# Performance work log

Hardware: AMD Instinct MI355X
Metric: run time of the kernel (lower is better)

## Reference

```python
import jax, jax.numpy as jnp
import numpy as np

B, S, T, H, VS, VT = 64, 64, 64, 1024, 32000, 32000


def _init(key, shape, scale=0.05):
    return scale * jax.random.normal(key, shape, dtype=jnp.float32)


def setup_inputs() -> dict:
    key = jax.random.key(0)
    ks = jax.random.split(key, 16)
    source = jax.random.randint(ks[0], (B, S), 0, VS)
    target = jax.random.randint(ks[1], (B, T), 0, VT)
    emb_src = _init(ks[2], (VS, H)).at[0].set(0.0)   # padding_idx=0
    emb_tgt = _init(ks[3], (VT, H)).at[0].set(0.0)   # padding_idx=0
    W_ih_enc = _init(ks[4], (4 * H, H)); W_hh_enc = _init(ks[5], (4 * H, H))
    b_ih_enc = _init(ks[6], (4 * H,));   b_hh_enc = _init(ks[7], (4 * H,))
    W_ih_dec = _init(ks[8], (4 * H, H)); W_hh_dec = _init(ks[9], (4 * H, H))
    b_ih_dec = _init(ks[10], (4 * H,));  b_hh_dec = _init(ks[11], (4 * H,))
    W_att = _init(ks[12], (H, 2 * H));   b_att = _init(ks[13], (H,))
    W_out = _init(ks[14], (VT, H));      b_out = _init(ks[15], (VT,))
    return dict(source=source, target=target, emb_src=emb_src, emb_tgt=emb_tgt,
                W_ih_enc=W_ih_enc, W_hh_enc=W_hh_enc, b_ih_enc=b_ih_enc, b_hh_enc=b_hh_enc,
                W_ih_dec=W_ih_dec, W_hh_dec=W_hh_dec, b_ih_dec=b_ih_dec, b_hh_dec=b_hh_dec,
                W_att=W_att, b_att=b_att, W_out=W_out, b_out=b_out)


def _lstm_cell(x, h, c, W_ih, W_hh, b):
    # PyTorch gate order: i, f, g, o
    gates = x @ W_ih.T + h @ W_hh.T + b
    i, f, g, o = jnp.split(gates, 4, axis=-1)
    c_new = jax.nn.sigmoid(f) * c + jax.nn.sigmoid(i) * jnp.tanh(g)
    h_new = jax.nn.sigmoid(o) * jnp.tanh(c_new)
    return h_new, c_new


def reference(source, target, emb_src, emb_tgt,
              W_ih_enc, W_hh_enc, b_ih_enc, b_hh_enc,
              W_ih_dec, W_hh_dec, b_ih_dec, b_hh_dec,
              W_att, b_att, W_out, b_out):
    src = source.T              # [S, B]
    tgt = target.T              # [T, B]
    h0 = jnp.zeros((B, H), jnp.float32)
    c0 = jnp.zeros((B, H), jnp.float32)

    # ---- Encoder: time-major LSTM via scan (dropout in eval mode = identity) ----
    x_src = emb_src[src]        # [S, B, H]
    b_enc = b_ih_enc + b_hh_enc

    def enc_step(carry, x_t):
        h, c = carry
        h, c = _lstm_cell(x_t, h, c, W_ih_enc, W_hh_enc, b_enc)
        return (h, c), h

    (hT, cT), hx_list = jax.lax.scan(enc_step, (h0, c0), x_src)  # hx_list: [S, B, H]

    # ---- Decoder: hx_cx is never updated in the original loop, so every
    # timestep uses the SAME encoder final state -> fully vectorizable over t ----
    words_f = tgt[: S - 1]      # [Td, B], Td = T-1 (S == T)
    words_t = tgt[1:]           # [Td, B]
    x_dec = emb_tgt[words_f]    # [Td, B, H]
    b_dec = b_ih_dec + b_hh_dec
    gates = x_dec @ W_ih_dec.T + (hT @ W_hh_dec.T + b_dec)[None]  # [Td, B, 4H]
    i, f, g, o = jnp.split(gates, 4, axis=-1)
    c_new = jax.nn.sigmoid(f) * cT[None] + jax.nn.sigmoid(i) * jnp.tanh(g)
    hx = jax.nn.sigmoid(o) * jnp.tanh(c_new)                       # [Td, B, H]

    # ---- Attention (dot-product over source positions, softmax over S) ----
    scores = jnp.einsum('tbh,sbh->tsb', hx, hx_list)               # [Td, S, B]
    neg_inf = jnp.asarray(-jnp.inf, jnp.float32)
    mask = (src != 0)[None]                                        # [1, S, B]
    scores = jnp.where(mask, scores, neg_inf)
    align = jax.nn.softmax(scores, axis=1)                         # over S
    content = jnp.einsum('tsb,sbh->tbh', align, hx_list)           # [Td, B, H]
    concat = jnp.concatenate([content, hx], axis=-1)               # [Td, B, 2H]
    hx_att = jnp.tanh(concat @ W_att.T + b_att)                    # [Td, B, H]

    # ---- Output projection + per-step cross entropy (ignore_index=0), summed ----
    logits = hx_att @ W_out.T + b_out                              # [Td, B, VT]
    logp = jax.nn.log_softmax(logits, axis=-1)
    nll = -jnp.take_along_axis(logp, words_t[..., None], axis=-1).squeeze(-1)  # [Td, B]
    valid = (words_t != 0).astype(jnp.float32)
    per_step = jnp.sum(nll * valid, axis=1) / jnp.maximum(jnp.sum(valid, axis=1), 1.0)
    return jnp.sum(per_step)
```

## Files before the change

kernel.cpp:

```cpp
#include <hip/hip_runtime.h>
#include <math.h>

#define Bb 64
#define Ss 64
#define Hh 1024
#define Vv 32000
#define RD 4032
#define RP 4096
#define NT4 4096
#define ENC_NBLK 128

typedef unsigned short u16;
typedef unsigned long long u64;
typedef __attribute__((ext_vector_type(8))) short bf16x8;
typedef __attribute__((ext_vector_type(4))) float f32x4;

#define MFMA(a, b, c) __builtin_amdgcn_mfma_f32_16x16x32_bf16(a, b, c, 0, 0, 0)

__device__ __forceinline__ u16 f2b(float f) {
  union { float f; unsigned u; } v; v.f = f;
  unsigned r = v.u + 0x7fffu + ((v.u >> 16) & 1u);
  return (u16)(r >> 16);
}
__device__ __forceinline__ float b2f(u16 b) {
  union { unsigned u; float f; } v; v.u = ((unsigned)b) << 16; return v.f;
}
__device__ __forceinline__ float sigf(float x) { return 1.f / (1.f + expf(-x)); }

__device__ __forceinline__ void gll16(const void* g, void* l) {
  __builtin_amdgcn_global_load_lds(
      (const __attribute__((address_space(1))) unsigned int*)g,
      (__attribute__((address_space(3))) unsigned int*)l, 16, 0, 0);
}

__global__ void k_fail(float* out) { out[0] = 1e30f; }

__global__ void k_cvt(const float* __restrict__ in, u16* __restrict__ out, int n4) {
  int i = blockIdx.x * blockDim.x + threadIdx.x;
  const int st = gridDim.x * blockDim.x;
  for (; i < n4; i += st) {
    float4 v = ((const float4*)in)[i];
    ushort4 o; o.x = f2b(v.x); o.y = f2b(v.y); o.z = f2b(v.z); o.w = f2b(v.w);
    ((ushort4*)out)[i] = o;
  }
}

__global__ void k_gather(const int* __restrict__ tok, const float* __restrict__ emb,
                         u16* __restrict__ outp, int nstep) {
  const int r = blockIdx.x;
  const int step = r >> 6, b = r & 63;
  const int idx = (step < nstep) ? tok[b * 64 + step] : 0;
  const float4 v = ((const float4*)(emb + (size_t)idx * Hh))[threadIdx.x];
  ushort4 o; o.x = f2b(v.x); o.y = f2b(v.y); o.z = f2b(v.z); o.w = f2b(v.w);
  ((ushort4*)(outp + (size_t)r * Hh))[threadIdx.x] = o;
}

template<int EPI>
__global__ __launch_bounds__(256)
void k_gemm(const u16* __restrict__ A, const u16* __restrict__ Bm,
            float* __restrict__ C, int M, int N, int K,
            const float* __restrict__ bias, int act,
            float* __restrict__ pmax, float* __restrict__ psum, int ncols) {
  __shared__ __align__(16) u16 As[128 * 64];
  __shared__ __align__(16) u16 Bs[128 * 64];
  const int tid = threadIdx.x;
  const int wave = tid >> 6, lane = tid & 63;
  const int l15 = lane & 15, lhi = lane >> 4;
  int bx = blockIdx.x, by = blockIdx.y;
  {
    const int nwg = gridDim.x * gridDim.y;
    if ((nwg & 7) == 0) {
      int flat = by * gridDim.x + bx;
      const int q = nwg >> 3;
      flat = (flat & 7) * q + (flat >> 3);
      bx = flat % gridDim.x; by = flat / gridDim.x;
    }
  }
  const int m0 = by * 128, n0 = bx * 128;
  const int wm = (wave >> 1) * 64, wn = (wave & 1) * 64;
  f32x4 acc[4][4] = {};

  const int srow = wave * 32 + (lane >> 3);
  const int scolb = (lane & 7) * 16;

  for (int k0 = 0; k0 < K; k0 += 64) {
    __syncthreads();
#pragma unroll
    for (int q = 0; q < 4; ++q) {
      const int r = srow + q * 8;
      int ra = m0 + r; ra = (ra < M) ? ra : (M - 1);
      const char* ga = (const char*)(A + (size_t)ra * K + k0) + scolb;
      const char* gb = (const char*)(Bm + (size_t)(n0 + r) * K + k0) + scolb;
      char* lA = (char*)As + (wave * 32 + q * 8) * 128;
      char* lB = (char*)Bs + (wave * 32 + q * 8) * 128;
      gll16(ga, lA);
      gll16(gb, lB);
    }
    __syncthreads();
#pragma unroll
    for (int kk = 0; kk < 2; ++kk) {
      const int ko = kk * 32 + lhi * 8;
      bf16x8 af[4], bfr[4];
#pragma unroll
      for (int i = 0; i < 4; ++i) af[i] = *(const bf16x8*)(As + (wm + i * 16 + l15) * 64 + ko);
#pragma unroll
      for (int j = 0; j < 4; ++j) bfr[j] = *(const bf16x8*)(Bs + (wn + j * 16 + l15) * 64 + ko);
#pragma unroll
      for (int i = 0; i < 4; ++i)
#pragma unroll
        for (int j = 0; j < 4; ++j)
          acc[i][j] = MFMA(af[i], bfr[j], acc[i][j]);
    }
  }

  if (EPI == 0) {
#pragma unroll
    for (int i = 0; i < 4; ++i) {
      const int gr = m0 + wm + i * 16 + lhi * 4;
#pragma unroll
      for (int j = 0; j < 4; ++j) {
        const int gc = n0 + wn + j * 16 + l15;
        const float bv = bias ? bias[gc] : 0.f;
#pragma unroll
        for (int rr = 0; rr < 4; ++rr) {
          float v = acc[i][j][rr] + bv;
          if (act) v = tanhf(v);
          C[(size_t)(gr + rr) * N + gc] = v;
        }
      }
    }
  } else {
    float bj[4];
#pragma unroll
    for (int j = 0; j < 4; ++j) bj[j] = bias[n0 + wn + j * 16 + l15];
    const int pc = bx * 2 + (wn ? 1 : 0);
#pragma unroll
    for (int i = 0; i < 4; ++i) {
#pragma unroll
      for (int rr = 0; rr < 4; ++rr) {
        float v0 = acc[i][0][rr] + bj[0];
        float v1 = acc[i][1][rr] + bj[1];
        float v2 = acc[i][2][rr] + bj[2];
        float v3 = acc[i][3][rr] + bj[3];
        float m = fmaxf(fmaxf(v0, v1), fmaxf(v2, v3));
#pragma unroll
        for (int d = 1; d < 16; d <<= 1) m = fmaxf(m, __shfl_xor(m, d, 64));
        float s = __expf(v0 - m) + __expf(v1 - m) + __expf(v2 - m) + __expf(v3 - m);
#pragma unroll
        for (int d = 1; d < 16; d <<= 1) s += __shfl_xor(s, d, 64);
        if (l15 == 0) {
          const int grow = m0 + wm + i * 16 + lhi * 4 + rr;
          pmax[(size_t)grow * ncols + pc] = m;
          psum[(size_t)grow * ncols + pc] = s;
        }
      }
    }
  }
}

__global__ __launch_bounds__(256, 1)
void k_enc_all(const u16* __restrict__ Wb, const float* __restrict__ gx,
               const float* __restrict__ b_ih, const float* __restrict__ b_hh,
               u16* __restrict__ hxl, float* __restrict__ c_out, int* flags) {
  __shared__ __align__(16) u16 Ws[32 * 1024];
  __shared__ float Gs[64 * 33];
  __shared__ float Cs[512];
  __shared__ float bsum[32];
  const int tid = threadIdx.x;
  const int wave = tid >> 6, lane = tid & 63;
  const int l15 = lane & 15, lhi = lane >> 4;
  const int c0 = blockIdx.x * 8;
  const int cb = tid >> 2, hp = (tid & 3) * 2;

  for (int i = tid; i < 32 * 128; i += 256) {
    const int rr = i >> 7, ck = i & 127;
    const int wrow = (rr >> 3) * Hh + c0 + (rr & 7);
    const int bo = (ck * 16) ^ ((rr & 7) << 4);
    *(bf16x8*)((char*)Ws + rr * 2048 + bo) = *(const bf16x8*)(Wb + (size_t)wrow * Hh + ck * 8);
  }
  if (tid < 32) {
    const int col = (tid >> 3) * Hh + c0 + (tid & 7);
    bsum[tid] = b_ih[col] + b_hh[col];
  }
  for (int i = tid; i < 512; i += 256) Cs[i] = 0.f;
  __syncthreads();

  for (int s = 0; s < 64; ++s) {
    const float* gp = gx + (size_t)(s * 64 + cb) * NT4 + c0 + hp;
    float g0[4], g1[4];
    g0[0] = gp[0];      g1[0] = gp[1];
    g0[1] = gp[Hh];     g1[1] = gp[Hh + 1];
    g0[2] = gp[2 * Hh]; g1[2] = gp[2 * Hh + 1];
    g0[3] = gp[3 * Hh]; g1[3] = gp[3 * Hh + 1];

    f32x4 a0a = {}, a0b = {}, a1a = {}, a1b = {};
    if (s > 0) {
      const u64* apw = (const u64*)(hxl + ((size_t)(s - 1) * 64 + wave * 16 + l15) * Hh);
      bf16x8 hf[32];
#pragma unroll
      for (int g = 0; g < 2; ++g) {
        for (;;) {
          const int f = __hip_atomic_load(flags + (g * 64 + lane) * 4,
                                          __ATOMIC_RELAXED, __HIP_MEMORY_SCOPE_AGENT);
          if (__all(f >= s)) break;
          __builtin_amdgcn_s_sleep(1);
        }
#pragma unroll
        for (int kf2 = 0; kf2 < 16; ++kf2) {
          const int kf = g * 16 + kf2;
          const int kw = (kf * 32 + lhi * 8) >> 2;
          const u64 q0 = __hip_atomic_load(apw + kw, __ATOMIC_RELAXED,
                                           __HIP_MEMORY_SCOPE_AGENT);
          const u64 q1 = __hip_atomic_load(apw + kw + 1, __ATOMIC_RELAXED,
                                           __HIP_MEMORY_SCOPE_AGENT);
          union { u64 q[2]; bf16x8 v; } cv;
          cv.q[0] = q0; cv.q[1] = q1;
          hf[kf] = cv.v;
        }
      }
      const char* wsb = (const char*)Ws;
      const int xr = (l15 & 7) << 4;
#pragma unroll
      for (int kf = 0; kf < 32; ++kf) {
        const int k = kf * 32 + lhi * 8;
        const int bo = (k * 2) ^ xr;
        const bf16x8 b0 = *(const bf16x8*)(wsb + l15 * 2048 + bo);
        const bf16x8 b1 = *(const bf16x8*)(wsb + (16 + l15) * 2048 + bo);
        if (kf & 1) { a0b = MFMA(hf[kf], b0, a0b); a1b = MFMA(hf[kf], b1, a1b); }
        else        { a0a = MFMA(hf[kf], b0, a0a); a1a = MFMA(hf[kf], b1, a1a); }
      }
    }
#pragma unroll
    for (int r = 0; r < 4; ++r) {
      Gs[(wave * 16 + lhi * 4 + r) * 33 + l15] = a0a[r] + a0b[r];
      Gs[(wave * 16 + lhi * 4 + r) * 33 + 16 + l15] = a1a[r] + a1b[r];
    }
    __syncthreads();
    {
      const int e0 = cb * 8 + hp;
      const float gi0 = Gs[cb * 33 + hp]          + g0[0] + bsum[hp];
      const float gf0 = Gs[cb * 33 + 8 + hp]      + g0[1] + bsum[8 + hp];
      const float gg0 = Gs[cb * 33 + 16 + hp]     + g0[2] + bsum[16 + hp];
      const float go0 = Gs[cb * 33 + 24 + hp]     + g0[3] + bsum[24 + hp];
      const float gi1 = Gs[cb * 33 + hp + 1]      + g1[0] + bsum[hp + 1];
      const float gf1 = Gs[cb * 33 + 8 + hp + 1]  + g1[1] + bsum[8 + hp + 1];
      const float gg1 = Gs[cb * 33 + 16 + hp + 1] + g1[2] + bsum[16 + hp + 1];
      const float go1 = Gs[cb * 33 + 24 + hp + 1] + g1[3] + bsum[24 + hp + 1];
      const float cn0 = sigf(gf0) * Cs[e0]     + sigf(gi0) * tanhf(gg0);
      const float cn1 = sigf(gf1) * Cs[e0 + 1] + sigf(gi1) * tanhf(gg1);
      const float hv0 = sigf(go0) * tanhf(cn0);
      const float hv1 = sigf(go1) * tanhf(cn1);
      Cs[e0] = cn0; Cs[e0 + 1] = cn1;
      const unsigned pk = (unsigned)f2b(hv0) | ((unsigned)f2b(hv1) << 16);
      __hip_atomic_store((unsigned*)(hxl + ((size_t)s * 64 + cb) * Hh + c0 + hp), pk,
                         __ATOMIC_RELAXED, __HIP_MEMORY_SCOPE_AGENT);
    }
    __syncthreads();
    if (tid == 0)
      __hip_atomic_store(flags + blockIdx.x * 4, s + 1,
                         __ATOMIC_RELAXED, __HIP_MEMORY_SCOPE_AGENT);
  }
  for (int e = tid; e < 512; e += 256)
    c_out[(e >> 3) * Hh + c0 + (e & 7)] = Cs[e];
}

__global__ void k_dec_cell(const float* __restrict__ G, const float* __restrict__ dbase,
                           const float* __restrict__ cT, const float* __restrict__ b_ih,
                           const float* __restrict__ b_hh, u16* __restrict__ Acat) {
  const int idx = blockIdx.x * 256 + threadIdx.x;
  if (idx >= RD * Hh) return;
  const int r = idx >> 10, nh = idx & 1023;
  const int b = r & 63;
  const size_t gr = (size_t)r * NT4;
  const size_t br = (size_t)b * NT4;
  const float gi = G[gr + nh]        + dbase[br + nh]        + b_ih[nh]        + b_hh[nh];
  const float gf = G[gr + Hh + nh]   + dbase[br + Hh + nh]   + b_ih[Hh + nh]   + b_hh[Hh + nh];
  const float gg = G[gr + 2*Hh + nh] + dbase[br + 2*Hh + nh] + b_ih[2*Hh + nh] + b_hh[2*Hh + nh];
  const float go = G[gr + 3*Hh + nh] + dbase[br + 3*Hh + nh] + b_ih[3*Hh + nh] + b_hh[3*Hh + nh];
  const float cn = sigf(gf) * cT[b * Hh + nh] + sigf(gi) * tanhf(gg);
  const float hv = sigf(go) * tanhf(cn);
  Acat[(size_t)r * 2048 + Hh + nh] = f2b(hv);
}

__global__ __launch_bounds__(256)
void k_attn(u16* Acat, const u16* __restrict__ hxl, const int* __restrict__ src) {
  __shared__ float qs[Hh];
  __shared__ float sc[Ss];
  const int r = blockIdx.x;
  const int b = r & 63;
  const int tid = threadIdx.x, wave = tid >> 6, lane = tid & 63;
  for (int h = tid; h < Hh; h += 256) qs[h] = b2f(Acat[(size_t)r * 2048 + Hh + h]);
  __syncthreads();
  for (int sub = 0; sub < 16; ++sub) {
    const int ss = wave * 16 + sub;
    const ushort4* hp4 = (const ushort4*)(hxl + ((size_t)ss * Bb + b) * Hh);
    float p = 0.f;
#pragma unroll
    for (int q = 0; q < 4; ++q) {
      const int i4 = lane + 64 * q;
      const ushort4 v = hp4[i4];
      p += qs[i4 * 4 + 0] * b2f(v.x) + qs[i4 * 4 + 1] * b2f(v.y)
         + qs[i4 * 4 + 2] * b2f(v.z) + qs[i4 * 4 + 3] * b2f(v.w);
    }
#pragma unroll
    for (int d = 1; d < 64; d <<= 1) p += __shfl_xor(p, d, 64);
    if (lane == 0) sc[ss] = (src[b * 64 + ss] != 0) ? p : -INFINITY;
  }
  __syncthreads();
  if (wave == 0) {
    const float v = sc[lane];
    float m = v;
#pragma unroll
    for (int d = 1; d < 64; d <<= 1) m = fmaxf(m, __shfl_xor(m, d, 64));
    const float e = __expf(v - m);
    float ssum = e;
#pragma unroll
    for (int d = 1; d < 64; d <<= 1) ssum += __shfl_xor(ssum, d, 64);
    sc[lane] = e / ssum;
  }
  __syncthreads();
  float4 a4 = {0.f, 0.f, 0.f, 0.f};
  for (int s2 = 0; s2 < 64; ++s2) {
    const float a = sc[s2];
    const ushort4 v = *(const ushort4*)(hxl + ((size_t)s2 * Bb + b) * Hh + tid * 4);
    a4.x += a * b2f(v.x); a4.y += a * b2f(v.y);
    a4.z += a * b2f(v.z); a4.w += a * b2f(v.w);
  }
  u16* dst = Acat + (size_t)r * 2048 + tid * 4;
  dst[0] = f2b(a4.x); dst[1] = f2b(a4.y); dst[2] = f2b(a4.z); dst[3] = f2b(a4.w);
}

__global__ void k_lse(const float* __restrict__ pmax, const float* __restrict__ psum,
                      float* __restrict__ lse, int ncols) {
  const int r = blockIdx.x * 4 + (threadIdx.x >> 6);
  const int lane = threadIdx.x & 63;
  if (r >= RD) return;
  float m = -INFINITY;
  for (int i = lane; i < ncols; i += 64) m = fmaxf(m, pmax[(size_t)r * ncols + i]);
#pragma unroll
  for (int d = 1; d < 64; d <<= 1) m = fmaxf(m, __shfl_xor(m, d, 64));
  float s = 0.f;
  for (int i = lane; i < ncols; i += 64)
    s += psum[(size_t)r * ncols + i] * __expf(pmax[(size_t)r * ncols + i] - m);
#pragma unroll
  for (int d = 1; d < 64; d <<= 1) s += __shfl_xor(s, d, 64);
  if (lane == 0) lse[r] = m + logf(s);
}

__global__ void k_tlogit(const float* __restrict__ hx_att, const int* __restrict__ target,
                         const float* __restrict__ W, const float* __restrict__ bo,
                         float* __restrict__ outp) {
  const int r = blockIdx.x * 4 + (threadIdx.x >> 6);
  const int lane = threadIdx.x & 63;
  if (r >= RD) return;
  const int t = r >> 6, b = r & 63;
  const int w = target[b * 64 + t + 1];
  const float* a = hx_att + (size_t)r * Hh;
  const float* wr = W + (size_t)w * Hh;
  float p = 0.f;
  for (int h = lane; h < Hh; h += 64) p += a[h] * wr[h];
#pragma unroll
  for (int d = 1; d < 64; d <<= 1) p += __shfl_xor(p, d, 64);
  if (lane == 0) outp[r] = p + bo[w];
}

__global__ void k_final(const float* __restrict__ lse, const float* __restrict__ tl,
                        const int* __restrict__ target, float* __restrict__ out) {
  const int t = threadIdx.x;
  float ps = 0.f;
  if (t < 63) {
    float sn = 0.f, cnt = 0.f;
    for (int b = 0; b < 64; ++b) {
      const int r = t * 64 + b;
      const int w = target[b * 64 + t + 1];
      if (w != 0) { sn += lse[r] - tl[r]; cnt += 1.f; }
    }
    ps = sn / fmaxf(cnt, 1.f);
  }
#pragma unroll
  for (int d = 1; d < 64; d <<= 1) ps += __shfl_xor(ps, d, 64);
  if (t == 0) out[0] = ps;
}

extern "C" void kernel_launch(void* const* d_in, const int* in_sizes, int n_in,
                              void* d_out, int out_size, void* d_ws, size_t ws_size,
                              hipStream_t stream) {
  const int*   source   = (const int*)d_in[0];
  const int*   target   = (const int*)d_in[1];
  const float* emb_src  = (const float*)d_in[2];
  const float* emb_tgt  = (const float*)d_in[3];
  const float* W_ih_enc = (const float*)d_in[4];
  const float* W_hh_enc = (const float*)d_in[5];
  const float* b_ih_enc = (const float*)d_in[6];
  const float* b_hh_enc = (const float*)d_in[7];
  const float* W_ih_dec = (const float*)d_in[8];
  const float* W_hh_dec = (const float*)d_in[9];
  const float* b_ih_dec = (const float*)d_in[10];
  const float* b_hh_dec = (const float*)d_in[11];
  const float* W_att    = (const float*)d_in[12];
  const float* b_att    = (const float*)d_in[13];
  const float* W_out    = (const float*)d_in[14];
  const float* b_out    = (const float*)d_in[15];
  float* out = (float*)d_out;

  char* base = (char*)d_ws;
  size_t off = 0;
  auto alloc = [&](size_t bytes) -> void* {
    void* r = base + off; off += (bytes + 255) & ~(size_t)255; return r;
  };
  u16*   wb_ih_enc = (u16*)alloc((size_t)NT4 * Hh * 2);
  u16*   wb_hh_enc = (u16*)alloc((size_t)NT4 * Hh * 2);
  u16*   wb_ih_dec = (u16*)alloc((size_t)NT4 * Hh * 2);
  u16*   wb_hh_dec = (u16*)alloc((size_t)NT4 * Hh * 2);
  u16*   wb_att    = (u16*)alloc((size_t)Hh * 2048 * 2);
  u16*   wb_out    = (u16*)alloc((size_t)Vv * Hh * 2);
  u16*   x_src_b   = (u16*)alloc((size_t)RP * Hh * 2);
  u16*   x_dec_b   = (u16*)alloc((size_t)RP * Hh * 2);
  float* gates     = (float*)alloc((size_t)RP * NT4 * 4);
  u16*   hxl       = (u16*)alloc((size_t)Ss * Bb * Hh * 2);
  float* c_enc     = (float*)alloc((size_t)Bb * Hh * 4);
  float* dbase     = (float*)alloc((size_t)128 * NT4 * 4);
  u16*   Acat      = (u16*)alloc((size_t)RP * 2048 * 2);
  float* hx_att    = (float*)alloc((size_t)RP * Hh * 4);
  u16*   hx_att_b  = (u16*)alloc((size_t)RP * Hh * 2);
  float* pmax      = (float*)alloc((size_t)RP * 500 * 4);
  float* psum      = (float*)alloc((size_t)RP * 500 * 4);
  float* lse       = (float*)alloc((size_t)RD * 4);
  float* tlog      = (float*)alloc((size_t)RD * 4);
  int*   flags     = (int*)alloc(ENC_NBLK * 16);

  if (off > ws_size) { k_fail<<<1, 1, 0, stream>>>(out); return; }

  k_cvt<<<2048, 256, 0, stream>>>(W_ih_enc, wb_ih_enc, NT4 * Hh / 4);
  k_cvt<<<2048, 256, 0, stream>>>(W_hh_enc, wb_hh_enc, NT4 * Hh / 4);
  k_cvt<<<2048, 256, 0, stream>>>(W_ih_dec, wb_ih_dec, NT4 * Hh / 4);
  k_cvt<<<2048, 256, 0, stream>>>(W_hh_dec, wb_hh_dec, NT4 * Hh / 4);
  k_cvt<<<2048, 256, 0, stream>>>(W_att, wb_att, Hh * 2048 / 4);
  k_cvt<<<2048, 256, 0, stream>>>(W_out, wb_out, Vv * Hh / 4);

  hipMemsetAsync(Acat, 0, (size_t)RP * 2048 * 2, stream);
  hipMemsetAsync(flags, 0, ENC_NBLK * 16, stream);

  k_gather<<<RP, 256, 0, stream>>>(source, emb_src, x_src_b, 64);
  k_gather<<<RP, 256, 0, stream>>>(target, emb_tgt, x_dec_b, 63);

  k_gemm<0><<<dim3(32, 32), 256, 0, stream>>>(x_src_b, wb_ih_enc, gates, RP, NT4, Hh,
                                              nullptr, 0, nullptr, nullptr, 0);
  k_enc_all<<<ENC_NBLK, 256, 0, stream>>>(wb_hh_enc, gates, b_ih_enc, b_hh_enc,
                                          hxl, c_enc, flags);

  k_gemm<0><<<dim3(32, 32), 256, 0, stream>>>(x_dec_b, wb_ih_dec, gates, RP, NT4, Hh,
                                              nullptr, 0, nullptr, nullptr, 0);
  k_gemm<0><<<dim3(32, 1), 256, 0, stream>>>(hxl + (size_t)63 * Bb * Hh, wb_hh_dec, dbase,
                                             64, NT4, Hh, nullptr, 0, nullptr, nullptr, 0);
  k_dec_cell<<<(RD * Hh) / 256, 256, 0, stream>>>(gates, dbase, c_enc, b_ih_dec, b_hh_dec, Acat);

  k_attn<<<RD, 256, 0, stream>>>(Acat, hxl, source);

  k_gemm<0><<<dim3(8, 32), 256, 0, stream>>>(Acat, wb_att, hx_att, RP, Hh, 2048,
                                             b_att, 1, nullptr, nullptr, 0);
  k_cvt<<<2048, 256, 0, stream>>>(hx_att, hx_att_b, RP * Hh / 4);

  k_gemm<2><<<dim3(250, 32), 256, 0, stream>>>(hx_att_b, wb_out, nullptr, RP, Vv, Hh,
                                               b_out, 0, pmax, psum, 500);
  k_lse<<<(RD + 3) / 4, 256, 0, stream>>>(pmax, psum, lse, 500);
  k_tlogit<<<(RD + 3) / 4, 256, 0, stream>>>(hx_att, target, W_out, b_out, tlog);
  k_final<<<1, 64, 0, stream>>>(lse, tlog, target, out);
}
```

Baseline: 1.551 ms.

## Halve encoder persistent blocks, add XCD-aware GEMM swizzle, drop Acat memset

The persistent encoder kernel now runs 64 blocks, each owning 16 hidden units (64 gate rows, 128KB of weights in LDS), instead of 128 blocks with 8 units each. The flag wait is done by one wave followed by a block barrier, and h fragments are loaded interleaved with the MFMAs using a per-block rotated k order. The cell state moves from shared memory to registers. The GEMM tile remap is changed to a 4x2 XCD-aware grouping, and the memset of Acat is removed, which assumes every used Acat region is written elsewhere. This trades fewer cross-block synchronisations per step against twice the serial MFMA work per block and higher LDS use.

```diff
diff --git a/kernel.cpp b/kernel.cpp
--- a/kernel.cpp
+++ b/kernel.cpp
@@ -8,7 +8,7 @@
 #define RD 4032
 #define RP 4096
 #define NT4 4096
-#define ENC_NBLK 128
+#define ENC_NBLK 64
 
 typedef unsigned short u16;
 typedef unsigned long long u64;
@@ -68,12 +68,19 @@
   const int l15 = lane & 15, lhi = lane >> 4;
   int bx = blockIdx.x, by = blockIdx.y;
   {
-    const int nwg = gridDim.x * gridDim.y;
-    if ((nwg & 7) == 0) {
-      int flat = by * gridDim.x + bx;
-      const int q = nwg >> 3;
-      flat = (flat & 7) * q + (flat >> 3);
-      bx = flat % gridDim.x; by = flat / gridDim.x;
+    const int gx_ = gridDim.x, gy_ = gridDim.y;
+    const int nwg = gx_ * gy_;
+    if ((gy_ & 3) == 0 && (gx_ & 1) == 0) {
+      const int f = by * gx_ + bx;
+      const int x = f & 7, i = f >> 3;
+      const int rby = gy_ >> 2, hx = gx_ >> 1;
+      by = (x >> 1) * rby + (i % rby);
+      bx = (x & 1) * hx + (i / rby);
+    } else if ((nwg & 7) == 0) {
+      int flat = by * gx_ + bx;
+      const int qq = nwg >> 3;
+      flat = (flat & 7) * qq + (flat >> 3);
+      bx = flat % gx_; by = flat / gx_;
     }
   }
   const int m0 = by * 128, n0 = bx * 128;
@@ -162,97 +169,89 @@
 void k_enc_all(const u16* __restrict__ Wb, const float* __restrict__ gx,
                const float* __restrict__ b_ih, const float* __restrict__ b_hh,
                u16* __restrict__ hxl, float* __restrict__ c_out, int* flags) {
-  __shared__ __align__(16) u16 Ws[32 * 1024];
-  __shared__ float Gs[64 * 33];
-  __shared__ float Cs[512];
-  __shared__ float bsum[32];
+  __shared__ __align__(16) u16 Ws[64 * 1024];
+  __shared__ float Gs[64 * 65];
+  __shared__ float bsum[64];
   const int tid = threadIdx.x;
   const int wave = tid >> 6, lane = tid & 63;
   const int l15 = lane & 15, lhi = lane >> 4;
-  const int c0 = blockIdx.x * 8;
-  const int cb = tid >> 2, hp = (tid & 3) * 2;
-
-  for (int i = tid; i < 32 * 128; i += 256) {
-    const int rr = i >> 7, ck = i & 127;
-    const int wrow = (rr >> 3) * Hh + c0 + (rr & 7);
-    const int bo = (ck * 16) ^ ((rr & 7) << 4);
-    *(bf16x8*)((char*)Ws + rr * 2048 + bo) = *(const bf16x8*)(Wb + (size_t)wrow * Hh + ck * 8);
-  }
-  if (tid < 32) {
-    const int col = (tid >> 3) * Hh + c0 + (tid & 7);
+  const int c0 = blockIdx.x * 16;
+  const int cb = tid >> 2, cq = tid & 3;
+  const int rot = blockIdx.x & 31;
+
+  for (int i = tid; i < 64 * 128; i += 256) {
+    const int r = i >> 7, ck = i & 127;
+    const int grow = (r >> 4) * Hh + c0 + (r & 15);
+    const int bo = (ck * 16) ^ ((r & 7) << 4);
+    *(bf16x8*)((char*)Ws + r * 2048 + bo) = *(const bf16x8*)(Wb + (size_t)grow * Hh + ck * 8);
+  }
+  if (tid < 64) {
+    const int col = (tid >> 4) * Hh + c0 + (tid & 15);
     bsum[tid] = b_ih[col] + b_hh[col];
   }
-  for (int i = tid; i < 512; i += 256) Cs[i] = 0.f;
+  float creg[4] = {0.f, 0.f, 0.f, 0.f};
   __syncthreads();
 
   for (int s = 0; s < 64; ++s) {
-    const float* gp = gx + (size_t)(s * 64 + cb) * NT4 + c0 + hp;
-    float g0[4], g1[4];
-    g0[0] = gp[0];      g1[0] = gp[1];
-    g0[1] = gp[Hh];     g1[1] = gp[Hh + 1];
-    g0[2] = gp[2 * Hh]; g1[2] = gp[2 * Hh + 1];
-    g0[3] = gp[3 * Hh]; g1[3] = gp[3 * Hh + 1];
-
-    f32x4 a0a = {}, a0b = {}, a1a = {}, a1b = {};
+    float4 ga[4];
+#pragma unroll
+    for (int g = 0; g < 4; ++g)
+      ga[g] = *(const float4*)(gx + (size_t)(s * 64 + cb) * NT4 + g * Hh + c0 + cq * 4);
+
+    f32x4 acc[4] = {};
     if (s > 0) {
-      const u64* apw = (const u64*)(hxl + ((size_t)(s - 1) * 64 + wave * 16 + l15) * Hh);
-      bf16x8 hf[32];
-#pragma unroll
-      for (int g = 0; g < 2; ++g) {
+      if (wave == 0) {
         for (;;) {
-          const int f = __hip_atomic_load(flags + (g * 64 + lane) * 4,
+          const int f = __hip_atomic_load(flags + lane * 4,
                                           __ATOMIC_RELAXED, __HIP_MEMORY_SCOPE_AGENT);
           if (__all(f >= s)) break;
           __builtin_amdgcn_s_sleep(1);
         }
-#pragma unroll
-        for (int kf2 = 0; kf2 < 16; ++kf2) {
-          const int kf = g * 16 + kf2;
-          const int kw = (kf * 32 + lhi * 8) >> 2;
-          const u64 q0 = __hip_atomic_load(apw + kw, __ATOMIC_RELAXED,
-                                           __HIP_MEMORY_SCOPE_AGENT);
-          const u64 q1 = __hip_atomic_load(apw + kw + 1, __ATOMIC_RELAXED,
-                                           __HIP_MEMORY_SCOPE_AGENT);
-          union { u64 q[2]; bf16x8 v; } cv;
-          cv.q[0] = q0; cv.q[1] = q1;
-          hf[kf] = cv.v;
+      }
+      __syncthreads();
+      const u64* apw = (const u64*)(hxl + ((size_t)(s - 1) * 64 + wave * 16 + l15) * Hh);
+      const char* wsb = (const char*)Ws;
+      const int xr = (l15 & 7) << 4;
+#pragma unroll 8
+      for (int i = 0; i < 32; ++i) {
+        const int kf = (i + rot) & 31;
+        const int k = kf * 32 + lhi * 8;
+        const u64 ua = __hip_atomic_load(apw + (k >> 2), __ATOMIC_RELAXED,
+                                         __HIP_MEMORY_SCOPE_AGENT);
+        const u64 ub = __hip_atomic_load(apw + (k >> 2) + 1, __ATOMIC_RELAXED,
+                                         __HIP_MEMORY_SCOPE_AGENT);
+        union { u64 qq[2]; bf16x8 v; } cv;
+        cv.qq[0] = ua; cv.qq[1] = ub;
+        const int kb = (k * 2) ^ xr;
+#pragma unroll
+        for (int nt = 0; nt < 4; ++nt) {
+          const bf16x8 bfrag = *(const bf16x8*)(wsb + (nt * 16 + l15) * 2048 + kb);
+          acc[nt] = MFMA(cv.v, bfrag, acc[nt]);
         }
       }
-      const char* wsb = (const char*)Ws;
-      const int xr = (l15 & 7) << 4;
-#pragma unroll
-      for (int kf = 0; kf < 32; ++kf) {
-        const int k = kf * 32 + lhi * 8;
-        const int bo = (k * 2) ^ xr;
-        const bf16x8 b0 = *(const bf16x8*)(wsb + l15 * 2048 + bo);
-        const bf16x8 b1 = *(const bf16x8*)(wsb + (16 + l15) * 2048 + bo);
-        if (kf & 1) { a0b = MFMA(hf[kf], b0, a0b); a1b = MFMA(hf[kf], b1, a1b); }
-        else        { a0a = MFMA(hf[kf], b0, a0a); a1a = MFMA(hf[kf], b1, a1a); }
-      }
-    }
-#pragma unroll
-    for (int r = 0; r < 4; ++r) {
-      Gs[(wave * 16 + lhi * 4 + r) * 33 + l15] = a0a[r] + a0b[r];
-      Gs[(wave * 16 + lhi * 4 + r) * 33 + 16 + l15] = a1a[r] + a1b[r];
-    }
+    }
+#pragma unroll
+    for (int nt = 0; nt < 4; ++nt)
+#pragma unroll
+      for (int r = 0; r < 4; ++r)
+        Gs[(wave * 16 + lhi * 4 + r) * 65 + nt * 16 + l15] = acc[nt][r];
     __syncthreads();
     {
-      const int e0 = cb * 8 + hp;
-      const float gi0 = Gs[cb * 33 + hp]          + g0[0] + bsum[hp];
-      const float gf0 = Gs[cb * 33 + 8 + hp]      + g0[1] + bsum[8 + hp];
-      const float gg0 = Gs[cb * 33 + 16 + hp]     + g0[2] + bsum[16 + hp];
-      const float go0 = Gs[cb * 33 + 24 + hp]     + g0[3] + bsum[24 + hp];
-      const float gi1 = Gs[cb * 33 + hp + 1]      + g1[0] + bsum[hp + 1];
-      const float gf1 = Gs[cb * 33 + 8 + hp + 1]  + g1[1] + bsum[8 + hp + 1];
-      const float gg1 = Gs[cb * 33 + 16 + hp + 1] + g1[2] + bsum[16 + hp + 1];
-      const float go1 = Gs[cb * 33 + 24 + hp + 1] + g1[3] + bsum[24 + hp + 1];
-      const float cn0 = sigf(gf0) * Cs[e0]     + sigf(gi0) * tanhf(gg0);
-      const float cn1 = sigf(gf1) * Cs[e0 + 1] + sigf(gi1) * tanhf(gg1);
-      const float hv0 = sigf(go0) * tanhf(cn0);
-      const float hv1 = sigf(go1) * tanhf(cn1);
-      Cs[e0] = cn0; Cs[e0 + 1] = cn1;
-      const unsigned pk = (unsigned)f2b(hv0) | ((unsigned)f2b(hv1) << 16);
-      __hip_atomic_store((unsigned*)(hxl + ((size_t)s * 64 + cb) * Hh + c0 + hp), pk,
+      const float* gsrow = Gs + cb * 65;
+      u64 pk = 0;
+#pragma unroll
+      for (int j = 0; j < 4; ++j) {
+        const int col = cq * 4 + j;
+        const float gi = gsrow[col]      + ga[0][j] + bsum[col];
+        const float gf = gsrow[16 + col] + ga[1][j] + bsum[16 + col];
+        const float gg = gsrow[32 + col] + ga[2][j] + bsum[32 + col];
+        const float go = gsrow[48 + col] + ga[3][j] + bsum[48 + col];
+        const float cn = sigf(gf) * creg[j] + sigf(gi) * tanhf(gg);
+        const float hv = sigf(go) * tanhf(cn);
+        creg[j] = cn;
+        pk |= (u64)f2b(hv) << (16 * j);
+      }
+      __hip_atomic_store((u64*)(hxl + ((size_t)s * 64 + cb) * Hh + c0 + cq * 4), pk,
                          __ATOMIC_RELAXED, __HIP_MEMORY_SCOPE_AGENT);
     }
     __syncthreads();
@@ -260,8 +259,9 @@
       __hip_atomic_store(flags + blockIdx.x * 4, s + 1,
                          __ATOMIC_RELAXED, __HIP_MEMORY_SCOPE_AGENT);
   }
-  for (int e = tid; e < 512; e += 256)
-    c_out[(e >> 3) * Hh + c0 + (e & 7)] = Cs[e];
+#pragma unroll
+  for (int j = 0; j < 4; ++j)
+    c_out[cb * Hh + c0 + cq * 4 + j] = creg[j];
 }
 
 __global__ void k_dec_cell(const float* __restrict__ G, const float* __restrict__ dbase,
@@ -438,7 +438,6 @@
   k_cvt<<<2048, 256, 0, stream>>>(W_att, wb_att, Hh * 2048 / 4);
   k_cvt<<<2048, 256, 0, stream>>>(W_out, wb_out, Vv * Hh / 4);
 
-  hipMemsetAsync(Acat, 0, (size_t)RP * 2048 * 2, stream);
   hipMemsetAsync(flags, 0, ENC_NBLK * 16, stream);
 
   k_gather<<<RP, 256, 0, stream>>>(source, emb_src, x_src_b, 64);
```

Measured after the change: 1.546 ms. Within noise of the previous version (-0.3%).
